# Optimization experiments

Hardware: AMD Instinct MI355X
Metric: run time of the kernel (lower is better)

The kernel has to match this reference:

```python
import jax, jax.numpy as jnp
import numpy as np

B, S, DM = 2, 2048, 1024
H, DH = 16, 64
SCALE = jnp.sqrt(jnp.float32(DH))  # dot_scale = sqrt(dim_head)


def setup_inputs() -> dict:
    key = jax.random.key(0)
    ks = jax.random.split(key, 9)
    std = 1.0 / np.sqrt(DM)
    x = jax.random.normal(ks[0], (B, S, DM), dtype=jnp.float32)
    Wq = jax.random.uniform(ks[1], (DM, DM), jnp.float32, -std, std)
    bq = jax.random.uniform(ks[2], (DM,), jnp.float32, -std, std)
    Wk = jax.random.uniform(ks[3], (DM, DM), jnp.float32, -std, std)
    bk = jax.random.uniform(ks[4], (DM,), jnp.float32, -std, std)
    Wv = jax.random.uniform(ks[5], (DM, DM), jnp.float32, -std, std)
    bv = jax.random.uniform(ks[6], (DM,), jnp.float32, -std, std)
    Wo = jax.random.uniform(ks[7], (DM, DM), jnp.float32, -std, std)
    bo = jax.random.uniform(ks[8], (DM,), jnp.float32, -std, std)
    # causal mask: 1 = masked (future positions), broadcast over batch
    causal = jnp.triu(jnp.ones((S, S), dtype=jnp.int32), k=1)
    attention_mask = jnp.broadcast_to(causal, (B, S, S))
    return {"x": x, "Wq": Wq, "bq": bq, "Wk": Wk, "bk": bk,
            "Wv": Wv, "bv": bv, "Wo": Wo, "bo": bo,
            "attention_mask": attention_mask}


def reference(x, Wq, bq, Wk, bk, Wv, bv, Wo, bo, attention_mask):
    # Linear layers (torch nn.Linear: y = x @ W^T + b)
    q = (x @ Wq.T + bq).reshape(B, S, H, DH).transpose(0, 2, 1, 3)  # (B,H,S,DH)
    k = (x @ Wk.T + bk).reshape(B, S, H, DH).transpose(0, 2, 1, 3)  # (B,H,S,DH)
    v = (x @ Wv.T + bv).reshape(B, S, H, DH).transpose(0, 2, 1, 3)  # (B,H,S,DH)
    # scores: (B,H,S,S), then mask==1 -> -inf, softmax over last dim
    scores = jnp.einsum('bhsd,bhtd->bhst', q, k) / SCALE
    mask = attention_mask[:, None, :, :]  # (B,1,S,S)
    scores = jnp.where(mask == 1, -jnp.inf, scores)
    attn = jax.nn.softmax(scores, axis=-1)
    # dropout is identity in eval mode
    ctx = jnp.einsum('bhst,bhtd->bshd', attn, v).reshape(B, S, H * DH)
    return ctx @ Wo.T + bo
```

## Files before the change

kernel.cpp:

```cpp
#include <hip/hip_runtime.h>
#include <stdint.h>

typedef unsigned short u16;
typedef __attribute__((ext_vector_type(8))) short bf16x8;
typedef __attribute__((ext_vector_type(4))) float f32x4;

#define BATCH 2
#define S_LEN 2048
#define DMODEL 1024
#define NH 16
#define DHEAD 64
#define MTOT 4096
#define QSCALE 0.18033688011112042f

#define GL2LDS(g, l) \
  __builtin_amdgcn_global_load_lds((const __attribute__((address_space(1))) void*)(g), \
                                   (__attribute__((address_space(3))) void*)(l), 16, 0, 0)

__device__ __forceinline__ u16 f2bf(float x) {
  union { float f; uint32_t u; } v; v.f = x;
  uint32_t r = v.u + 0x7fffu + ((v.u >> 16) & 1u);
  return (u16)(r >> 16);
}
__device__ __forceinline__ u16 f2bf_fast(float x) {
  union { float f; uint32_t u; } v; v.f = x;
  return (u16)((v.u + 0x8000u) >> 16);
}

struct CvtArgs {
  const float* src[5];
  u16* dst[5];
};

__global__ __launch_bounds__(256) void cvt_all(CvtArgs a) {
  int bx = blockIdx.x;
  int region, off;
  if (bx < 4096) { region = 0; off = bx; }
  else { region = 1 + ((bx - 4096) >> 10); off = (bx - 4096) & 1023; }
  const float* s = a.src[region];
  u16* d = a.dst[region];
  int i = (off * 256 + threadIdx.x) * 4;
  float4 v = *(const float4*)(s + i);
  uint2 pk;
  pk.x = (uint32_t)f2bf(v.x) | ((uint32_t)f2bf(v.y) << 16);
  pk.y = (uint32_t)f2bf(v.z) | ((uint32_t)f2bf(v.w) << 16);
  *(uint2*)(d + i) = pk;
}

__device__ __forceinline__ void gemm_body(const u16* __restrict__ A,
                                          const u16* __restrict__ W,
                                          const float* __restrict__ bias,
                                          void* __restrict__ out,
                                          int mode, float scale) {
  __shared__ u16 As[128 * 32];
  __shared__ u16 Bs[128 * 32];
  const int tid = threadIdx.x;
  const int m0 = blockIdx.y * 128;
  const int n0 = blockIdx.x * 128;
  const int wave = tid >> 6, lane = tid & 63;
  const int wm = (wave >> 1) * 64, wn = (wave & 1) * 64;
  const int quad = lane >> 4, l15 = lane & 15;

  const int row0 = tid >> 2, g0 = ((tid & 3) ^ (row0 & 3)) * 8;
  const int row1 = (tid + 256) >> 2, g1 = ((tid & 3) ^ (row1 & 3)) * 8;
  const int lb0 = wave * 512;
  const int lb1 = 2048 + wave * 512;
  const int xk = (quad ^ (l15 & 3)) * 8;

  f32x4 acc[4][4] = {};

  for (int kt = 0; kt < DMODEL; kt += 32) {
    GL2LDS(A + (size_t)(m0 + row0) * DMODEL + kt + g0, As + lb0);
    GL2LDS(A + (size_t)(m0 + row1) * DMODEL + kt + g1, As + lb1);
    GL2LDS(W + (size_t)(n0 + row0) * DMODEL + kt + g0, Bs + lb0);
    GL2LDS(W + (size_t)(n0 + row1) * DMODEL + kt + g1, Bs + lb1);
    __syncthreads();
    bf16x8 af[4], bfr[4];
#pragma unroll
    for (int bi = 0; bi < 4; ++bi)
      af[bi] = *(const bf16x8*)(&As[(wm + bi * 16 + l15) * 32 + xk]);
#pragma unroll
    for (int bj = 0; bj < 4; ++bj)
      bfr[bj] = *(const bf16x8*)(&Bs[(wn + bj * 16 + l15) * 32 + xk]);
#pragma unroll
    for (int bi = 0; bi < 4; ++bi)
#pragma unroll
      for (int bj = 0; bj < 4; ++bj)
        acc[bi][bj] = __builtin_amdgcn_mfma_f32_16x16x32_bf16(af[bi], bfr[bj], acc[bi][bj], 0, 0, 0);
    __syncthreads();
  }

#pragma unroll
  for (int bi = 0; bi < 4; ++bi) {
#pragma unroll
    for (int bj = 0; bj < 4; ++bj) {
      int n = n0 + wn + bj * 16 + l15;
      float bval = bias[n];
#pragma unroll
      for (int r = 0; r < 4; ++r) {
        int m = m0 + wm + bi * 16 + quad * 4 + r;
        float v = (acc[bi][bj][r] + bval) * scale;
        u16 bvu = f2bf(v);
        int b = m >> 11, s = m & 2047;
        int h = n >> 6, d = n & 63;
        size_t bh = (size_t)(b * NH + h);
        if (mode == 1)
          ((u16*)out)[(bh * S_LEN + s) * DHEAD + d] = bvu;
        else
          ((u16*)out)[((bh * 256 + (s >> 3)) * 64 + d) * 8 + (s & 7)] = bvu;
      }
    }
  }
}

struct QKVArgs {
  const u16* w[3];
  const float* b[3];
  u16* o[3];
};

__global__ __launch_bounds__(256) void qkv_gemm(const u16* __restrict__ xb, QKVArgs a) {
  int z = blockIdx.z;
  int mode = (z == 2) ? 2 : 1;
  float scale = (z == 0) ? QSCALE : 1.0f;
  gemm_body(xb, a.w[z], a.b[z], a.o[z], mode, scale);
}

__global__ __launch_bounds__(256) void out_gemm(const u16* __restrict__ A,
                                                const u16* __restrict__ W,
                                                const float* __restrict__ bias,
                                                float* __restrict__ out) {
  __shared__ u16 As[128 * 32];
  __shared__ u16 Bs[64 * 32];
  const int tid = threadIdx.x;
  const int m0 = blockIdx.y * 128;
  const int n0 = blockIdx.x * 64;
  const int wave = tid >> 6, lane = tid & 63;
  const int wm = (wave >> 1) * 64, wn = (wave & 1) * 32;
  const int quad = lane >> 4, l15 = lane & 15;

  const int row0 = tid >> 2, g0 = ((tid & 3) ^ (row0 & 3)) * 8;
  const int row1 = (tid + 256) >> 2, g1 = ((tid & 3) ^ (row1 & 3)) * 8;
  const int lb0 = wave * 512;
  const int lb1 = 2048 + wave * 512;
  const int xk = (quad ^ (l15 & 3)) * 8;

  f32x4 acc[4][2] = {};

  for (int kt = 0; kt < DMODEL; kt += 32) {
    GL2LDS(A + (size_t)(m0 + row0) * DMODEL + kt + g0, As + lb0);
    GL2LDS(A + (size_t)(m0 + row1) * DMODEL + kt + g1, As + lb1);
    GL2LDS(W + (size_t)(n0 + row0) * DMODEL + kt + g0, Bs + lb0);
    __syncthreads();
    bf16x8 af[4], bfr[2];
#pragma unroll
    for (int bi = 0; bi < 4; ++bi)
      af[bi] = *(const bf16x8*)(&As[(wm + bi * 16 + l15) * 32 + xk]);
#pragma unroll
    for (int bj = 0; bj < 2; ++bj)
      bfr[bj] = *(const bf16x8*)(&Bs[(wn + bj * 16 + l15) * 32 + xk]);
#pragma unroll
    for (int bi = 0; bi < 4; ++bi)
#pragma unroll
      for (int bj = 0; bj < 2; ++bj)
        acc[bi][bj] = __builtin_amdgcn_mfma_f32_16x16x32_bf16(af[bi], bfr[bj], acc[bi][bj], 0, 0, 0);
    __syncthreads();
  }

#pragma unroll
  for (int bi = 0; bi < 4; ++bi) {
#pragma unroll
    for (int bj = 0; bj < 2; ++bj) {
      int n = n0 + wn + bj * 16 + l15;
      float bval = bias[n];
#pragma unroll
      for (int r = 0; r < 4; ++r) {
        int m = m0 + wm + bi * 16 + quad * 4 + r;
        out[(size_t)m * DMODEL + n] = acc[bi][bj][r] + bval;
      }
    }
  }
}

__global__ __launch_bounds__(256, 4) void attn(const u16* __restrict__ Q,
                                               const u16* __restrict__ Kg,
                                               const u16* __restrict__ Vt8,
                                               u16* __restrict__ ctx) {
  __shared__ u16 Kd[2][64 * 64];
  __shared__ u16 Vd[2][64 * 64];
  __shared__ u16 Ps[64 * 64];
  const int tid = threadIdx.x;
  const int g = blockIdx.x >> 5;
  const int bh = blockIdx.x & 31;
  const int gv = g & 7;
  int qt = (g & 8) ? (15 - gv) : gv;
  if (g & 16) qt += 16;
  const int wave = tid >> 6, lane = tid & 63;
  const int quad = lane >> 4, l15 = lane & 15;
  const size_t base = (size_t)bh * S_LEN * DHEAD;
  const int b = bh >> 4, h = bh & 15;
  const int xk7 = l15 & 7;

#define STAGE(kt_, pb)                                                                   \
  do {                                                                                   \
    _Pragma("unroll")                                                                    \
    for (int i_ = 0; i_ < 2; ++i_) {                                                     \
      int c_ = tid + 256 * i_;                                                           \
      int row_ = c_ >> 3, g_ = ((c_ & 7) ^ (row_ & 7)) * 8;                              \
      GL2LDS(Kg + base + (size_t)((kt_) * 64 + row_) * 64 + g_,                          \
             &Kd[pb][0] + i_ * 2048 + wave * 512);                                       \
      GL2LDS(Vt8 + base + (size_t)((kt_) * 512 + c_) * 8,                                \
             &Vd[pb][0] + i_ * 2048 + wave * 512);                                       \
    }                                                                                    \
  } while (0)

  const int qrow = qt * 64 + wave * 16 + l15;
  bf16x8 qf0 = *(const bf16x8*)(Q + base + (size_t)qrow * DHEAD + quad * 8);
  bf16x8 qf1 = *(const bf16x8*)(Q + base + (size_t)qrow * DHEAD + 32 + quad * 8);

  float l_part[4] = {0.f, 0.f, 0.f, 0.f};
  f32x4 o[4] = {};

  STAGE(0, 0);

  for (int kt = 0; kt <= qt; ++kt) {
    const int p = kt & 1;
    __syncthreads();
    if (kt < qt) STAGE(kt + 1, p ^ 1);

    const bool diag = (kt == qt);
    f32x4 s_acc[4];
#pragma unroll
    for (int bj = 0; bj < 4; ++bj) {
      if (diag && bj > wave) {
        s_acc[bj] = f32x4{-1e30f, -1e30f, -1e30f, -1e30f};
        continue;
      }
      const int krow = (bj * 16 + l15) * 64;
      bf16x8 kf0 = *(const bf16x8*)(&Kd[p][krow + ((quad ^ xk7) * 8)]);
      bf16x8 kf1 = *(const bf16x8*)(&Kd[p][krow + (((quad + 4) ^ xk7) * 8)]);
      f32x4 t = {0.f, 0.f, 0.f, 0.f};
      t = __builtin_amdgcn_mfma_f32_16x16x32_bf16(qf0, kf0, t, 0, 0, 0);
      t = __builtin_amdgcn_mfma_f32_16x16x32_bf16(qf1, kf1, t, 0, 0, 0);
      s_acc[bj] = t;
    }

    if (diag) {
#pragma unroll
      for (int bj = 0; bj < 4; ++bj) {
        int kg = kt * 64 + bj * 16 + l15;
#pragma unroll
        for (int r = 0; r < 4; ++r) {
          int qg = qt * 64 + wave * 16 + quad * 4 + r;
          if (kg > qg) s_acc[bj][r] = -1e30f;
        }
      }
    }

#pragma unroll
    for (int bj = 0; bj < 4; ++bj) {
#pragma unroll
      for (int r = 0; r < 4; ++r) {
        float pv = exp2f(s_acc[bj][r]);
        l_part[r] += pv;
        int row = wave * 16 + quad * 4 + r;
        int ch = (bj * 2 + (l15 >> 3)) ^ (row & 7);
        Ps[row * 64 + ch * 8 + (l15 & 7)] = f2bf_fast(pv);
      }
    }

    {
      const int row2 = wave * 16 + l15;
#pragma unroll
      for (int kk = 0; kk < 2; ++kk) {
        bf16x8 pf = *(const bf16x8*)(&Ps[row2 * 64 + (((kk << 2) + quad) ^ xk7) * 8]);
#pragma unroll
        for (int dj = 0; dj < 4; ++dj) {
          bf16x8 vf = *(const bf16x8*)(&Vd[p][((kk * 4 + quad) * 64 + dj * 16 + l15) * 8]);
          o[dj] = __builtin_amdgcn_mfma_f32_16x16x32_bf16(pf, vf, o[dj], 0, 0, 0);
        }
      }
    }
  }

#pragma unroll
  for (int r = 0; r < 4; ++r) {
    float s = l_part[r];
    s += __shfl_xor(s, 1, 64);
    s += __shfl_xor(s, 2, 64);
    s += __shfl_xor(s, 4, 64);
    s += __shfl_xor(s, 8, 64);
    float inv = 1.0f / s;
    int srow = qt * 64 + wave * 16 + quad * 4 + r;
    size_t rowbase = ((size_t)b * S_LEN + srow) * DMODEL + h * DHEAD;
#pragma unroll
    for (int dj = 0; dj < 4; ++dj)
      ctx[rowbase + dj * 16 + l15] = f2bf(o[dj][r] * inv);
  }
#undef STAGE
}

extern "C" void kernel_launch(void* const* d_in, const int* in_sizes, int n_in,
                              void* d_out, int out_size, void* d_ws, size_t ws_size,
                              hipStream_t stream) {
  const float* x  = (const float*)d_in[0];
  const float* Wq = (const float*)d_in[1];
  const float* bq = (const float*)d_in[2];
  const float* Wk = (const float*)d_in[3];
  const float* bk = (const float*)d_in[4];
  const float* Wv = (const float*)d_in[5];
  const float* bv = (const float*)d_in[6];
  const float* Wo = (const float*)d_in[7];
  const float* bo = (const float*)d_in[8];
  float* out = (float*)d_out;

  char* ws = (char*)d_ws;
  const size_t MB = 1u << 20;
  u16* xb   = (u16*)(ws + 0);
  u16* ctxb = xb;
  u16* wqb  = (u16*)(ws + 8 * MB);
  u16* wkb  = (u16*)(ws + 10 * MB);
  u16* wvb  = (u16*)(ws + 12 * MB);
  u16* wob  = (u16*)(ws + 14 * MB);
  u16* qb   = (u16*)(ws + 16 * MB);
  u16* kb   = (u16*)(ws + 24 * MB);
  u16* vtb  = (u16*)(ws + 32 * MB);

  CvtArgs c;
  c.src[0] = x;  c.dst[0] = xb;
  c.src[1] = Wq; c.dst[1] = wqb;
  c.src[2] = Wk; c.dst[2] = wkb;
  c.src[3] = Wv; c.dst[3] = wvb;
  c.src[4] = Wo; c.dst[4] = wob;
  cvt_all<<<4096 + 4 * 1024, 256, 0, stream>>>(c);

  QKVArgs a;
  a.w[0] = wqb; a.w[1] = wkb; a.w[2] = wvb;
  a.b[0] = bq;  a.b[1] = bk;  a.b[2] = bv;
  a.o[0] = qb;  a.o[1] = kb;  a.o[2] = vtb;
  qkv_gemm<<<dim3(DMODEL / 128, MTOT / 128, 3), 256, 0, stream>>>(xb, a);

  attn<<<1024, 256, 0, stream>>>(qb, kb, vtb, ctxb);

  out_gemm<<<dim3(DMODEL / 64, MTOT / 128), 256, 0, stream>>>(ctxb, wob, bo, out);
}
```

Baseline: 210.0 us.

## Balance causal attention by pairing query tiles and splitting long rows

```diff
diff --git a/kernel.cpp b/kernel.cpp
--- a/kernel.cpp
+++ b/kernel.cpp
@@ -185,21 +185,22 @@
 __global__ __launch_bounds__(256, 4) void attn(const u16* __restrict__ Q,
                                                const u16* __restrict__ Kg,
                                                const u16* __restrict__ Vt8,
-                                               u16* __restrict__ ctx) {
+                                               u16* __restrict__ ctx,
+                                               float* __restrict__ part_o,
+                                               float* __restrict__ part_l) {
   __shared__ u16 Kd[2][64 * 64];
   __shared__ u16 Vd[2][64 * 64];
   __shared__ u16 Ps[64 * 64];
   const int tid = threadIdx.x;
-  const int g = blockIdx.x >> 5;
+  const int qp = blockIdx.x >> 6;
+  const int hh = (blockIdx.x >> 5) & 1;
   const int bh = blockIdx.x & 31;
-  const int gv = g & 7;
-  int qt = (g & 8) ? (15 - gv) : gv;
-  if (g & 16) qt += 16;
   const int wave = tid >> 6, lane = tid & 63;
   const int quad = lane >> 4, l15 = lane & 15;
   const size_t base = (size_t)bh * S_LEN * DHEAD;
   const int b = bh >> 4, h = bh & 15;
   const int xk7 = l15 & 7;
+  const int pidx = qp * 32 + bh;
 
 #define STAGE(kt_, pb)                                                                   \
   do {                                                                                   \
@@ -214,90 +215,133 @@
     }                                                                                    \
   } while (0)
 
-  const int qrow = qt * 64 + wave * 16 + l15;
-  bf16x8 qf0 = *(const bf16x8*)(Q + base + (size_t)qrow * DHEAD + quad * 8);
-  bf16x8 qf1 = *(const bf16x8*)(Q + base + (size_t)qrow * DHEAD + 32 + quad * 8);
-
-  float l_part[4] = {0.f, 0.f, 0.f, 0.f};
-  f32x4 o[4] = {};
-
-  STAGE(0, 0);
-
-  for (int kt = 0; kt <= qt; ++kt) {
-    const int p = kt & 1;
-    __syncthreads();
-    if (kt < qt) STAGE(kt + 1, p ^ 1);
-
-    const bool diag = (kt == qt);
-    f32x4 s_acc[4];
-#pragma unroll
-    for (int bj = 0; bj < 4; ++bj) {
-      if (diag && bj > wave) {
-        s_acc[bj] = f32x4{-1e30f, -1e30f, -1e30f, -1e30f};
-        continue;
-      }
-      const int krow = (bj * 16 + l15) * 64;
-      bf16x8 kf0 = *(const bf16x8*)(&Kd[p][krow + ((quad ^ xk7) * 8)]);
-      bf16x8 kf1 = *(const bf16x8*)(&Kd[p][krow + (((quad + 4) ^ xk7) * 8)]);
-      f32x4 t = {0.f, 0.f, 0.f, 0.f};
-      t = __builtin_amdgcn_mfma_f32_16x16x32_bf16(qf0, kf0, t, 0, 0, 0);
-      t = __builtin_amdgcn_mfma_f32_16x16x32_bf16(qf1, kf1, t, 0, 0, 0);
-      s_acc[bj] = t;
+  const int nph = hh ? 1 : 2;
+  for (int ph = 0; ph < nph; ++ph) {
+    int qt, k0, k1, pmode;
+    if (hh == 0 && ph == 0) { qt = qp;      k0 = 0;       k1 = qp;      pmode = 0; }
+    else if (hh == 0)       { qt = 31 - qp; k0 = 0;       k1 = 15 - qp; pmode = 1; }
+    else                    { qt = 31 - qp; k0 = 16 - qp; k1 = 31 - qp; pmode = 1; }
+
+    const int qrow = qt * 64 + wave * 16 + l15;
+    bf16x8 qf0 = *(const bf16x8*)(Q + base + (size_t)qrow * DHEAD + quad * 8);
+    bf16x8 qf1 = *(const bf16x8*)(Q + base + (size_t)qrow * DHEAD + 32 + quad * 8);
+
+    float l_part[4] = {0.f, 0.f, 0.f, 0.f};
+    f32x4 o[4] = {};
+
+    STAGE(k0, 0);
+
+    for (int kt = k0; kt <= k1; ++kt) {
+      const int p = (kt - k0) & 1;
+      __syncthreads();
+      if (kt < k1) STAGE(kt + 1, p ^ 1);
+
+      const bool diag = (kt == qt);
+      f32x4 s_acc[4];
+#pragma unroll
+      for (int bj = 0; bj < 4; ++bj) {
+        if (diag && bj > wave) {
+          s_acc[bj] = f32x4{-1e30f, -1e30f, -1e30f, -1e30f};
+          continue;
+        }
+        const int krow = (bj * 16 + l15) * 64;
+        bf16x8 kf0 = *(const bf16x8*)(&Kd[p][krow + ((quad ^ xk7) * 8)]);
+        bf16x8 kf1 = *(const bf16x8*)(&Kd[p][krow + (((quad + 4) ^ xk7) * 8)]);
+        f32x4 t = {0.f, 0.f, 0.f, 0.f};
+        t = __builtin_amdgcn_mfma_f32_16x16x32_bf16(qf0, kf0, t, 0, 0, 0);
+        t = __builtin_amdgcn_mfma_f32_16x16x32_bf16(qf1, kf1, t, 0, 0, 0);
+        s_acc[bj] = t;
+      }
+
+      if (diag) {
+#pragma unroll
+        for (int bj = 0; bj < 4; ++bj) {
+          int kg = kt * 64 + bj * 16 + l15;
+#pragma unroll
+          for (int r = 0; r < 4; ++r) {
+            int qg = qt * 64 + wave * 16 + quad * 4 + r;
+            if (kg > qg) s_acc[bj][r] = -1e30f;
+          }
+        }
+      }
+
+#pragma unroll
+      for (int bj = 0; bj < 4; ++bj) {
+#pragma unroll
+        for (int r = 0; r < 4; ++r) {
+          float pv = exp2f(s_acc[bj][r]);
+          l_part[r] += pv;
+          int row = wave * 16 + quad * 4 + r;
+          int ch = (bj * 2 + (l15 >> 3)) ^ (row & 7);
+          Ps[row * 64 + ch * 8 + (l15 & 7)] = f2bf_fast(pv);
+        }
+      }
+
+      {
+        const int row2 = wave * 16 + l15;
+#pragma unroll
+        for (int kk = 0; kk < 2; ++kk) {
+          bf16x8 pf = *(const bf16x8*)(&Ps[row2 * 64 + (((kk << 2) + quad) ^ xk7) * 8]);
+#pragma unroll
+          for (int dj = 0; dj < 4; ++dj) {
+            bf16x8 vf = *(const bf16x8*)(&Vd[p][((kk * 4 + quad) * 64 + dj * 16 + l15) * 8]);
+            o[dj] = __builtin_amdgcn_mfma_f32_16x16x32_bf16(pf, vf, o[dj], 0, 0, 0);
+          }
+        }
+      }
     }
 
-    if (diag) {
-#pragma unroll
-      for (int bj = 0; bj < 4; ++bj) {
-        int kg = kt * 64 + bj * 16 + l15;
-#pragma unroll
-        for (int r = 0; r < 4; ++r) {
-          int qg = qt * 64 + wave * 16 + quad * 4 + r;
-          if (kg > qg) s_acc[bj][r] = -1e30f;
-        }
+    __syncthreads();
+
+#pragma unroll
+    for (int r = 0; r < 4; ++r) {
+      float s = l_part[r];
+      s += __shfl_xor(s, 1, 64);
+      s += __shfl_xor(s, 2, 64);
+      s += __shfl_xor(s, 4, 64);
+      s += __shfl_xor(s, 8, 64);
+      int row = wave * 16 + quad * 4 + r;
+      if (pmode == 0) {
+        float inv = 1.0f / s;
+        int srow = qt * 64 + row;
+        size_t rowbase = ((size_t)b * S_LEN + srow) * DMODEL + h * DHEAD;
+#pragma unroll
+        for (int dj = 0; dj < 4; ++dj)
+          ctx[rowbase + dj * 16 + l15] = f2bf(o[dj][r] * inv);
+      } else {
+        float* po = part_o + ((size_t)hh * 512 + pidx) * 4096 + (size_t)row * 64;
+#pragma unroll
+        for (int dj = 0; dj < 4; ++dj)
+          po[dj * 16 + l15] = o[dj][r];
+        if (l15 == 0) part_l[((size_t)hh * 512 + pidx) * 64 + row] = s;
       }
     }
-
-#pragma unroll
-    for (int bj = 0; bj < 4; ++bj) {
-#pragma unroll
-      for (int r = 0; r < 4; ++r) {
-        float pv = exp2f(s_acc[bj][r]);
-        l_part[r] += pv;
-        int row = wave * 16 + quad * 4 + r;
-        int ch = (bj * 2 + (l15 >> 3)) ^ (row & 7);
-        Ps[row * 64 + ch * 8 + (l15 & 7)] = f2bf_fast(pv);
-      }
-    }
-
-    {
-      const int row2 = wave * 16 + l15;
-#pragma unroll
-      for (int kk = 0; kk < 2; ++kk) {
-        bf16x8 pf = *(const bf16x8*)(&Ps[row2 * 64 + (((kk << 2) + quad) ^ xk7) * 8]);
-#pragma unroll
-        for (int dj = 0; dj < 4; ++dj) {
-          bf16x8 vf = *(const bf16x8*)(&Vd[p][((kk * 4 + quad) * 64 + dj * 16 + l15) * 8]);
-          o[dj] = __builtin_amdgcn_mfma_f32_16x16x32_bf16(pf, vf, o[dj], 0, 0, 0);
-        }
-      }
-    }
-  }
-
-#pragma unroll
-  for (int r = 0; r < 4; ++r) {
-    float s = l_part[r];
-    s += __shfl_xor(s, 1, 64);
-    s += __shfl_xor(s, 2, 64);
-    s += __shfl_xor(s, 4, 64);
-    s += __shfl_xor(s, 8, 64);
-    float inv = 1.0f / s;
-    int srow = qt * 64 + wave * 16 + quad * 4 + r;
-    size_t rowbase = ((size_t)b * S_LEN + srow) * DMODEL + h * DHEAD;
-#pragma unroll
-    for (int dj = 0; dj < 4; ++dj)
-      ctx[rowbase + dj * 16 + l15] = f2bf(o[dj][r] * inv);
   }
 #undef STAGE
+}
+
+__global__ __launch_bounds__(256) void combine(const float* __restrict__ part_o,
+                                               const float* __restrict__ part_l,
+                                               u16* __restrict__ ctx) {
+  const int pidx = blockIdx.x;
+  const int qp = pidx >> 5, bh = pidx & 31;
+  const int qt = 31 - qp;
+  const int b = bh >> 4, h = bh & 15;
+  const float* poA = part_o + (size_t)pidx * 4096;
+  const float* poB = part_o + (512 + (size_t)pidx) * 4096;
+  const float* plA = part_l + (size_t)pidx * 64;
+  const float* plB = part_l + (512 + (size_t)pidx) * 64;
+  for (int i = threadIdx.x * 4; i < 4096; i += 1024) {
+    int row = i >> 6, col = i & 63;
+    float4 oa = *(const float4*)(poA + i);
+    float4 ob = *(const float4*)(poB + i);
+    float inv = 1.0f / (plA[row] + plB[row]);
+    uint2 pk;
+    pk.x = (uint32_t)f2bf((oa.x + ob.x) * inv) | ((uint32_t)f2bf((oa.y + ob.y) * inv) << 16);
+    pk.y = (uint32_t)f2bf((oa.z + ob.z) * inv) | ((uint32_t)f2bf((oa.w + ob.w) * inv) << 16);
+    int srow = qt * 64 + row;
+    *(uint2*)(ctx + ((size_t)b * S_LEN + srow) * DMODEL + h * DHEAD + col) = pk;
+  }
 }
 
 extern "C" void kernel_launch(void* const* d_in, const int* in_sizes, int n_in,
@@ -325,6 +369,8 @@
   u16* qb   = (u16*)(ws + 16 * MB);
   u16* kb   = (u16*)(ws + 24 * MB);
   u16* vtb  = (u16*)(ws + 32 * MB);
+  float* part_o = (float*)d_out;
+  float* part_l = (float*)(ws + 8 * MB);
 
   CvtArgs c;
   c.src[0] = x;  c.dst[0] = xb;
@@ -340,7 +386,9 @@
   a.o[0] = qb;  a.o[1] = kb;  a.o[2] = vtb;
   qkv_gemm<<<dim3(DMODEL / 128, MTOT / 128, 3), 256, 0, stream>>>(xb, a);
 
-  attn<<<1024, 256, 0, stream>>>(qb, kb, vtb, ctxb);
+  attn<<<1024, 256, 0, stream>>>(qb, kb, vtb, ctxb, part_o, part_l);
+
+  combine<<<512, 256, 0, stream>>>(part_o, part_l, ctxb);
 
   out_gemm<<<dim3(DMODEL / 64, MTOT / 128), 256, 0, stream>>>(ctxb, wob, bo, out);
 }
```

New measurement: 214.5 us. 1.02x slower.

## Double-buffer LDS in projection GEMMs and remap blocks per XCD for L2 locality

Applied to the files above, without the earlier changes.

```diff
diff --git a/kernel.cpp b/kernel.cpp
--- a/kernel.cpp
+++ b/kernel.cpp
@@ -51,12 +51,11 @@
                                           const u16* __restrict__ W,
                                           const float* __restrict__ bias,
                                           void* __restrict__ out,
-                                          int mode, float scale) {
-  __shared__ u16 As[128 * 32];
-  __shared__ u16 Bs[128 * 32];
+                                          int mode, float scale,
+                                          int m0, int n0) {
+  __shared__ u16 As[2][128 * 32];
+  __shared__ u16 Bs[2][128 * 32];
   const int tid = threadIdx.x;
-  const int m0 = blockIdx.y * 128;
-  const int n0 = blockIdx.x * 128;
   const int wave = tid >> 6, lane = tid & 63;
   const int wm = (wave >> 1) * 64, wn = (wave & 1) * 64;
   const int quad = lane >> 4, l15 = lane & 15;
@@ -69,26 +68,33 @@
 
   f32x4 acc[4][4] = {};
 
-  for (int kt = 0; kt < DMODEL; kt += 32) {
-    GL2LDS(A + (size_t)(m0 + row0) * DMODEL + kt + g0, As + lb0);
-    GL2LDS(A + (size_t)(m0 + row1) * DMODEL + kt + g1, As + lb1);
-    GL2LDS(W + (size_t)(n0 + row0) * DMODEL + kt + g0, Bs + lb0);
-    GL2LDS(W + (size_t)(n0 + row1) * DMODEL + kt + g1, Bs + lb1);
+#define GSTAGE(kt_, pb)                                                     \
+  do {                                                                      \
+    GL2LDS(A + (size_t)(m0 + row0) * DMODEL + (kt_) + g0, &As[pb][0] + lb0);\
+    GL2LDS(A + (size_t)(m0 + row1) * DMODEL + (kt_) + g1, &As[pb][0] + lb1);\
+    GL2LDS(W + (size_t)(n0 + row0) * DMODEL + (kt_) + g0, &Bs[pb][0] + lb0);\
+    GL2LDS(W + (size_t)(n0 + row1) * DMODEL + (kt_) + g1, &Bs[pb][0] + lb1);\
+  } while (0)
+
+  GSTAGE(0, 0);
+  for (int t = 0; t < 32; ++t) {
+    const int p = t & 1;
     __syncthreads();
+    if (t < 31) GSTAGE((t + 1) * 32, p ^ 1);
     bf16x8 af[4], bfr[4];
 #pragma unroll
     for (int bi = 0; bi < 4; ++bi)
-      af[bi] = *(const bf16x8*)(&As[(wm + bi * 16 + l15) * 32 + xk]);
+      af[bi] = *(const bf16x8*)(&As[p][(wm + bi * 16 + l15) * 32 + xk]);
 #pragma unroll
     for (int bj = 0; bj < 4; ++bj)
-      bfr[bj] = *(const bf16x8*)(&Bs[(wn + bj * 16 + l15) * 32 + xk]);
+      bfr[bj] = *(const bf16x8*)(&Bs[p][(wn + bj * 16 + l15) * 32 + xk]);
 #pragma unroll
     for (int bi = 0; bi < 4; ++bi)
 #pragma unroll
       for (int bj = 0; bj < 4; ++bj)
         acc[bi][bj] = __builtin_amdgcn_mfma_f32_16x16x32_bf16(af[bi], bfr[bj], acc[bi][bj], 0, 0, 0);
-    __syncthreads();
-  }
+  }
+#undef GSTAGE
 
 #pragma unroll
   for (int bi = 0; bi < 4; ++bi) {
@@ -119,22 +125,30 @@
   u16* o[3];
 };
 
-__global__ __launch_bounds__(256) void qkv_gemm(const u16* __restrict__ xb, QKVArgs a) {
-  int z = blockIdx.z;
+__global__ __launch_bounds__(256, 3) void qkv_gemm(const u16* __restrict__ xb, QKVArgs a) {
+  int s = blockIdx.x;
+  int xcd = s & 7, idx = s >> 3;
+  int xx = idx & 3, yy = (idx >> 2) & 7, z = idx >> 5;
+  int nt = (xcd & 1) * 4 + xx;
+  int mt = (xcd >> 1) * 8 + yy;
   int mode = (z == 2) ? 2 : 1;
   float scale = (z == 0) ? QSCALE : 1.0f;
-  gemm_body(xb, a.w[z], a.b[z], a.o[z], mode, scale);
-}
-
-__global__ __launch_bounds__(256) void out_gemm(const u16* __restrict__ A,
-                                                const u16* __restrict__ W,
-                                                const float* __restrict__ bias,
-                                                float* __restrict__ out) {
-  __shared__ u16 As[128 * 32];
-  __shared__ u16 Bs[64 * 32];
+  gemm_body(xb, a.w[z], a.b[z], a.o[z], mode, scale, mt * 128, nt * 128);
+}
+
+__global__ __launch_bounds__(256, 3) void out_gemm(const u16* __restrict__ A,
+                                                   const u16* __restrict__ W,
+                                                   const float* __restrict__ bias,
+                                                   float* __restrict__ out) {
+  int sb = blockIdx.x;
+  int xcd = sb & 7, idx = sb >> 3;
+  int xx = idx & 7, yy = idx >> 3;
+  const int n0 = ((xcd & 1) * 8 + xx) * 64;
+  const int m0 = ((xcd >> 1) * 8 + yy) * 128;
+
+  __shared__ u16 As[2][128 * 32];
+  __shared__ u16 Bs[2][64 * 32];
   const int tid = threadIdx.x;
-  const int m0 = blockIdx.y * 128;
-  const int n0 = blockIdx.x * 64;
   const int wave = tid >> 6, lane = tid & 63;
   const int wm = (wave >> 1) * 64, wn = (wave & 1) * 32;
   const int quad = lane >> 4, l15 = lane & 15;
@@ -147,25 +161,32 @@
 
   f32x4 acc[4][2] = {};
 
-  for (int kt = 0; kt < DMODEL; kt += 32) {
-    GL2LDS(A + (size_t)(m0 + row0) * DMODEL + kt + g0, As + lb0);
-    GL2LDS(A + (size_t)(m0 + row1) * DMODEL + kt + g1, As + lb1);
-    GL2LDS(W + (size_t)(n0 + row0) * DMODEL + kt + g0, Bs + lb0);
+#define OSTAGE(kt_, pb)                                                     \
+  do {                                                                      \
+    GL2LDS(A + (size_t)(m0 + row0) * DMODEL + (kt_) + g0, &As[pb][0] + lb0);\
+    GL2LDS(A + (size_t)(m0 + row1) * DMODEL + (kt_) + g1, &As[pb][0] + lb1);\
+    GL2LDS(W + (size_t)(n0 + row0) * DMODEL + (kt_) + g0, &Bs[pb][0] + lb0);\
+  } while (0)
+
+  OSTAGE(0, 0);
+  for (int t = 0; t < 32; ++t) {
+    const int p = t & 1;
     __syncthreads();
+    if (t < 31) OSTAGE((t + 1) * 32, p ^ 1);
     bf16x8 af[4], bfr[2];
 #pragma unroll
     for (int bi = 0; bi < 4; ++bi)
-      af[bi] = *(const bf16x8*)(&As[(wm + bi * 16 + l15) * 32 + xk]);
+      af[bi] = *(const bf16x8*)(&As[p][(wm + bi * 16 + l15) * 32 + xk]);
 #pragma unroll
     for (int bj = 0; bj < 2; ++bj)
-      bfr[bj] = *(const bf16x8*)(&Bs[(wn + bj * 16 + l15) * 32 + xk]);
+      bfr[bj] = *(const bf16x8*)(&Bs[p][(wn + bj * 16 + l15) * 32 + xk]);
 #pragma unroll
     for (int bi = 0; bi < 4; ++bi)
 #pragma unroll
       for (int bj = 0; bj < 2; ++bj)
         acc[bi][bj] = __builtin_amdgcn_mfma_f32_16x16x32_bf16(af[bi], bfr[bj], acc[bi][bj], 0, 0, 0);
-    __syncthreads();
-  }
+  }
+#undef OSTAGE
 
 #pragma unroll
   for (int bi = 0; bi < 4; ++bi) {
@@ -338,9 +359,9 @@
   a.w[0] = wqb; a.w[1] = wkb; a.w[2] = wvb;
   a.b[0] = bq;  a.b[1] = bk;  a.b[2] = bv;
   a.o[0] = qb;  a.o[1] = kb;  a.o[2] = vtb;
-  qkv_gemm<<<dim3(DMODEL / 128, MTOT / 128, 3), 256, 0, stream>>>(xb, a);
+  qkv_gemm<<<768, 256, 0, stream>>>(xb, a);
 
   attn<<<1024, 256, 0, stream>>>(qb, kb, vtb, ctxb);
 
-  out_gemm<<<dim3(DMODEL / 64, MTOT / 128), 256, 0, stream>>>(ctxb, wob, bo, out);
-}
+  out_gemm<<<512, 256, 0, stream>>>(ctxb, wob, bo, out);
+}
```

Result: no change. 208.6 us (-0.7%).
